# Kernel tuning notes

Hardware: AMD Instinct MI355X
Metric: run time of the kernel (lower is better)

Reference implementation:

```python
import jax, jax.numpy as jnp
import numpy as np

B, T, H = 2, 512, 256


def setup_inputs() -> dict:
    key = jax.random.key(0)
    k1, k2, k3, k4, k5 = jax.random.split(key, 5)
    scale = 1.0 / np.sqrt(H)
    Q = jax.random.normal(k1, (B, T, H), dtype=jnp.float32)
    K = jax.random.normal(k2, (B, T, H), dtype=jnp.float32)
    # torch nn.Linear weights: y = x @ W.T, W shape [out, in]
    Wq = jax.random.normal(k3, (H, H), dtype=jnp.float32) * scale
    Wk = jax.random.normal(k4, (H, H), dtype=jnp.float32) * scale
    v = jax.random.normal(k5, (H,), dtype=jnp.float32) * scale  # Linear(H,1) weight
    return {"Q": Q, "K": K, "Wq": Wq, "Wk": Wk, "v": v}


def reference(Q, K, Wq, Wk, v):
    # Project queries and keys: [B,T,H]
    Qp = jnp.einsum("bth,oh->bto", Q, Wq)
    Kp = jnp.einsum("bsh,oh->bso", K, Wk)
    # Additive (Bahdanau) scores: tanh over broadcast sum -> [B,T,T,H], then v-proj -> [B,T,T]
    e = jnp.tanh(Qp[:, :, None, :] + Kp[:, None, :, :])
    scores = jnp.einsum("btsh,h->bts", e, v)
    # Causal mask: query t may only attend to keys s <= t
    mask = jnp.tril(jnp.ones((T, T), dtype=bool))
    scores = jnp.where(mask[None, :, :], scores, jnp.float32(-1e9))
    alpha = jax.nn.softmax(scores, axis=-1)
    # Weighted sum of (raw) K values: [B,T,H]
    ctx = jnp.einsum("bts,bsh->bth", alpha, K)
    return ctx, alpha
```

## Files before the change

### kernel.cpp

```cpp
#include <hip/hip_runtime.h>

#define BB 2
#define TT 512
#define HH 256
#define NBT (BB * TT)

#define C2LOG2E 2.8853900817779268f
#define LOG2E   1.4426950408889634f

typedef __attribute__((ext_vector_type(8))) short short8;
typedef __attribute__((ext_vector_type(4))) float f32x4;

__device__ __forceinline__ unsigned short f2bf(float f) {
    unsigned u = __float_as_uint(f);
    unsigned r = u + 0x7fffu + ((u >> 16) & 1u);
    return (unsigned short)(r >> 16);
}

__device__ __forceinline__ short8 load_cvt8(const float* __restrict__ p) {
    float4 x0 = *reinterpret_cast<const float4*>(p);
    float4 x1 = *reinterpret_cast<const float4*>(p + 4);
    short8 r;
    r[0] = (short)f2bf(x0.x); r[1] = (short)f2bf(x0.y);
    r[2] = (short)f2bf(x0.z); r[3] = (short)f2bf(x0.w);
    r[4] = (short)f2bf(x1.x); r[5] = (short)f2bf(x1.y);
    r[6] = (short)f2bf(x1.z); r[7] = (short)f2bf(x1.w);
    return r;
}

__global__ __launch_bounds__(256) void proj_mfma_kernel(
    const float* __restrict__ Q, const float* __restrict__ K,
    const float* __restrict__ Wq, const float* __restrict__ Wk,
    float* __restrict__ Eq, float* __restrict__ EkT)
{
    int wid_g = blockIdx.x * 4 + (threadIdx.x >> 6);
    int lane = threadIdx.x & 63;
    int btile = wid_g >> 4;
    int otile = wid_g & 15;
    bool isK = (btile >= 64);
    int bt0 = (btile & 63) * 16;
    int o0 = otile * 16;
    const float* X = isK ? K : Q;
    const float* W = isK ? Wk : Wq;

    int rsel = lane & 15;
    int ksel = (lane >> 4) * 8;

    const float* xp = X + (bt0 + rsel) * HH + ksel;
    const float* wp = W + (o0 + rsel) * HH + ksel;

    f32x4 acc = {0.f, 0.f, 0.f, 0.f};
#pragma unroll 2
    for (int kb = 0; kb < 8; ++kb) {
        short8 a = load_cvt8(xp + kb * 32);
        short8 b = load_cvt8(wp + kb * 32);
        acc = __builtin_amdgcn_mfma_f32_16x16x32_bf16(a, b, acc, 0, 0, 0);
    }

    int rbase = bt0 + (lane >> 4) * 4;
    int o = o0 + (lane & 15);
#pragma unroll
    for (int j = 0; j < 4; ++j) {
        float e = __builtin_amdgcn_exp2f(acc[j] * C2LOG2E);
        int r = rbase + j;
        if (!isK)
            Eq[r * HH + o] = e;
        else
            EkT[((o >> 2) * NBT + r) * 4 + (o & 3)] = e;
    }
}

__global__ __launch_bounds__(512, 8) void attn_kernel(
    const float* __restrict__ Eq, const float* __restrict__ EkT,
    const float* __restrict__ Kraw, const float* __restrict__ v,
    float* __restrict__ ctx, float* __restrict__ alpha)
{
    __shared__ float eq_sh[HH];
    __shared__ float v2_sh[HH];
    __shared__ float al_sh[TT];
    __shared__ float red[8];
    __shared__ float4 cred[8][64];

    int bt = blockIdx.x;
    int b = bt / TT;
    int idx = bt % TT;
    int t = (idx < 256) ? idx : 767 - idx;
    int btr = b * TT + t;
    int tid = threadIdx.x;

    if (tid < HH) {
        eq_sh[tid] = Eq[btr * HH + tid];
        v2_sh[tid] = -2.0f * v[tid];
    }
    __syncthreads();

    float sc = 0.f;
    if (tid <= t) {
        const float4* ek = reinterpret_cast<const float4*>(EkT) + (b * TT + tid);
        const float4* q4p = reinterpret_cast<const float4*>(eq_sh);
        const float4* v4p = reinterpret_cast<const float4*>(v2_sh);
#pragma unroll 4
        for (int h4 = 0; h4 < HH / 4; ++h4) {
            float4 e4 = ek[h4 * NBT];
            float4 q4 = q4p[h4];
            float4 vv = v4p[h4];
            float r0 = __builtin_amdgcn_rcpf(__builtin_fmaf(q4.x, e4.x, 1.f));
            float r1 = __builtin_amdgcn_rcpf(__builtin_fmaf(q4.y, e4.y, 1.f));
            float r2 = __builtin_amdgcn_rcpf(__builtin_fmaf(q4.z, e4.z, 1.f));
            float r3 = __builtin_amdgcn_rcpf(__builtin_fmaf(q4.w, e4.w, 1.f));
            sc = __builtin_fmaf(vv.x, r0, sc);
            sc = __builtin_fmaf(vv.y, r1, sc);
            sc = __builtin_fmaf(vv.z, r2, sc);
            sc = __builtin_fmaf(vv.w, r3, sc);
        }
    }

    float e = (tid <= t) ? __builtin_amdgcn_exp2f(sc * LOG2E) : 0.f;
    float ssum = e;
#pragma unroll
    for (int off = 32; off > 0; off >>= 1)
        ssum += __shfl_xor(ssum, off);
    if ((tid & 63) == 0) red[tid >> 6] = ssum;
    __syncthreads();
    float denom = (red[0] + red[1]) + (red[2] + red[3])
                + (red[4] + red[5]) + (red[6] + red[7]);
    float a0 = e * __builtin_amdgcn_rcpf(denom);

    al_sh[tid] = a0;
    alpha[btr * TT + tid] = a0;
    __syncthreads();

    int hc = tid & 63, sg = tid >> 6;
    const float4* kb4 = reinterpret_cast<const float4*>(Kraw + b * TT * HH) + hc;
    float4 acc4 = {0.f, 0.f, 0.f, 0.f};
    for (int s = sg; s <= t; s += 8) {
        float4 k4 = kb4[s * 64];
        float  al = al_sh[s];
        acc4.x = __builtin_fmaf(al, k4.x, acc4.x);
        acc4.y = __builtin_fmaf(al, k4.y, acc4.y);
        acc4.z = __builtin_fmaf(al, k4.z, acc4.z);
        acc4.w = __builtin_fmaf(al, k4.w, acc4.w);
    }
    cred[sg][hc] = acc4;
    __syncthreads();
    if (sg == 0) {
        float4 out = {0.f, 0.f, 0.f, 0.f};
#pragma unroll
        for (int g = 0; g < 8; ++g) {
            float4 cc = cred[g][hc];
            out.x += cc.x; out.y += cc.y; out.z += cc.z; out.w += cc.w;
        }
        reinterpret_cast<float4*>(ctx + btr * HH)[hc] = out;
    }
}

extern "C" void kernel_launch(void* const* d_in, const int* in_sizes, int n_in,
                              void* d_out, int out_size, void* d_ws, size_t ws_size,
                              hipStream_t stream) {
    const float* Q  = (const float*)d_in[0];
    const float* K  = (const float*)d_in[1];
    const float* Wq = (const float*)d_in[2];
    const float* Wk = (const float*)d_in[3];
    const float* v  = (const float*)d_in[4];

    float* ctx   = (float*)d_out;
    float* alpha = (float*)d_out + NBT * HH;

    float* Eq  = (float*)d_ws;
    float* EkT = Eq + NBT * HH;

    proj_mfma_kernel<<<512, 256, 0, stream>>>(Q, K, Wq, Wk, Eq, EkT);
    attn_kernel<<<NBT, 512, 0, stream>>>(Eq, EkT, K, v, ctx, alpha);
}
```

Baseline: 37.51 us.

## Fuse projection and attention kernels with a global atomic grid barrier

```diff
diff --git a/kernel.cpp b/kernel.cpp
--- a/kernel.cpp
+++ b/kernel.cpp
@@ -28,65 +28,77 @@
     return r;
 }
 
-__global__ __launch_bounds__(256) void proj_mfma_kernel(
+__global__ __launch_bounds__(512, 8) void fused_kernel(
     const float* __restrict__ Q, const float* __restrict__ K,
     const float* __restrict__ Wq, const float* __restrict__ Wk,
-    float* __restrict__ Eq, float* __restrict__ EkT)
+    const float* __restrict__ v,
+    float* __restrict__ ctx, float* __restrict__ alpha,
+    float* __restrict__ Eq, float* __restrict__ EkT,
+    unsigned* __restrict__ cnt)
 {
-    int wid_g = blockIdx.x * 4 + (threadIdx.x >> 6);
-    int lane = threadIdx.x & 63;
-    int btile = wid_g >> 4;
-    int otile = wid_g & 15;
-    bool isK = (btile >= 64);
-    int bt0 = (btile & 63) * 16;
-    int o0 = otile * 16;
-    const float* X = isK ? K : Q;
-    const float* W = isK ? Wk : Wq;
+    int tid = threadIdx.x;
+    int bid = blockIdx.x;
+    int wv = tid >> 6;
 
-    int rsel = lane & 15;
-    int ksel = (lane >> 4) * 8;
+    if (wv < 2) {
+        int tileid = bid * 2 + wv;
+        int lane = tid & 63;
+        int btile = tileid >> 4;
+        int otile = tileid & 15;
+        bool isK = (btile >= 64);
+        int bt0 = (btile & 63) * 16;
+        int o0 = otile * 16;
+        const float* X = isK ? K : Q;
+        const float* W = isK ? Wk : Wq;
 
-    const float* xp = X + (bt0 + rsel) * HH + ksel;
-    const float* wp = W + (o0 + rsel) * HH + ksel;
+        int rsel = lane & 15;
+        int ksel = (lane >> 4) * 8;
+        const float* xp = X + (bt0 + rsel) * HH + ksel;
+        const float* wp = W + (o0 + rsel) * HH + ksel;
 
-    f32x4 acc = {0.f, 0.f, 0.f, 0.f};
+        f32x4 acc = {0.f, 0.f, 0.f, 0.f};
 #pragma unroll 2
-    for (int kb = 0; kb < 8; ++kb) {
-        short8 a = load_cvt8(xp + kb * 32);
-        short8 b = load_cvt8(wp + kb * 32);
-        acc = __builtin_amdgcn_mfma_f32_16x16x32_bf16(a, b, acc, 0, 0, 0);
+        for (int kb = 0; kb < 8; ++kb) {
+            short8 a = load_cvt8(xp + kb * 32);
+            short8 b = load_cvt8(wp + kb * 32);
+            acc = __builtin_amdgcn_mfma_f32_16x16x32_bf16(a, b, acc, 0, 0, 0);
+        }
+
+        int rbase = bt0 + (lane >> 4) * 4;
+        int o = o0 + (lane & 15);
+#pragma unroll
+        for (int j = 0; j < 4; ++j) {
+            float e = __builtin_amdgcn_exp2f(acc[j] * C2LOG2E);
+            int r = rbase + j;
+            if (!isK)
+                Eq[r * HH + o] = e;
+            else
+                EkT[((o >> 2) * NBT + r) * 4 + (o & 3)] = e;
+        }
     }
 
-    int rbase = bt0 + (lane >> 4) * 4;
-    int o = o0 + (lane & 15);
-#pragma unroll
-    for (int j = 0; j < 4; ++j) {
-        float e = __builtin_amdgcn_exp2f(acc[j] * C2LOG2E);
-        int r = rbase + j;
-        if (!isK)
-            Eq[r * HH + o] = e;
-        else
-            EkT[((o >> 2) * NBT + r) * 4 + (o & 3)] = e;
+    __syncthreads();
+    if (tid == 0) {
+        __threadfence();
+        atomicAdd(cnt, 1u);
+        while (atomicAdd(cnt, 0u) < (unsigned)NBT) {
+            __builtin_amdgcn_s_sleep(2);
+        }
+        __threadfence();
     }
-}
+    __syncthreads();
 
-__global__ __launch_bounds__(512, 8) void attn_kernel(
-    const float* __restrict__ Eq, const float* __restrict__ EkT,
-    const float* __restrict__ Kraw, const float* __restrict__ v,
-    float* __restrict__ ctx, float* __restrict__ alpha)
-{
     __shared__ float eq_sh[HH];
     __shared__ float v2_sh[HH];
     __shared__ float al_sh[TT];
     __shared__ float red[8];
     __shared__ float4 cred[8][64];
 
-    int bt = blockIdx.x;
+    int bt = bid;
     int b = bt / TT;
     int idx = bt % TT;
     int t = (idx < 256) ? idx : 767 - idx;
     int btr = b * TT + t;
-    int tid = threadIdx.x;
 
     if (tid < HH) {
         eq_sh[tid] = Eq[btr * HH + tid];
@@ -131,7 +143,7 @@
     __syncthreads();
 
     int hc = tid & 63, sg = tid >> 6;
-    const float4* kb4 = reinterpret_cast<const float4*>(Kraw + b * TT * HH) + hc;
+    const float4* kb4 = reinterpret_cast<const float4*>(K + b * TT * HH) + hc;
     float4 acc4 = {0.f, 0.f, 0.f, 0.f};
     for (int s = sg; s <= t; s += 8) {
         float4 k4 = kb4[s * 64];
@@ -168,7 +180,9 @@
 
     float* Eq  = (float*)d_ws;
     float* EkT = Eq + NBT * HH;
+    unsigned* cnt = (unsigned*)(EkT + NBT * HH);
 
-    proj_mfma_kernel<<<512, 256, 0, stream>>>(Q, K, Wq, Wk, Eq, EkT);
-    attn_kernel<<<NBT, 512, 0, stream>>>(Eq, EkT, K, v, ctx, alpha);
+    hipMemsetAsync((void*)cnt, 0, 4, stream);
+    fused_kernel<<<NBT, 512, 0, stream>>>(Q, K, Wq, Wk, v,
+                                          ctx, alpha, Eq, EkT, cnt);
 }
```

Result: slower. 147.2 us (+292.3%).
